# Optimization experiments

Measured on AMD Instinct MI355X. Metric: run time of the kernel, lower is better.

Reference implementation:

```python
import jax, jax.numpy as jnp
import numpy as np

NUM_RBF = 16
MAX_REL = 32          # max_relative_feature
AUTOREGRESSIVE = True
D_MIN, D_MAX = 2.0, 22.0
LN_EPS = 1e-5


def setup_inputs() -> dict:
    key = jax.random.key(0)
    ks = jax.random.split(key, 6)
    B, L, A, K = 1, 1280, 14, 30
    E_feat, edge_in = 128, 16 + NUM_RBF * 4 * 10  # 656
    X = jax.random.normal(ks[0], (B, L, A, 3), dtype=jnp.float32) * 3.0
    residue_idx = jnp.tile(jnp.arange(L, dtype=jnp.int32)[None], (B, 1))
    chain_labels = jnp.zeros((B, L), dtype=jnp.int32)
    E_idx = jax.random.randint(ks[1], (B, L, K), 0, L, dtype=jnp.int32)
    atom_mask = jnp.ones((B, L, A), dtype=jnp.float32)
    W_pos = jax.random.normal(ks[2], (2 * MAX_REL + 2, 16), dtype=jnp.float32) * 0.1
    b_pos = jnp.zeros((16,), dtype=jnp.float32)
    W_edge = jax.random.normal(ks[3], (edge_in, E_feat), dtype=jnp.float32) * 0.05
    ln_gamma = jnp.ones((E_feat,), dtype=jnp.float32)
    ln_beta = jnp.zeros((E_feat,), dtype=jnp.float32)
    return {"X": X, "residue_idx": residue_idx, "chain_labels": chain_labels,
            "E_idx": E_idx, "atom_mask": atom_mask, "W_pos": W_pos,
            "b_pos": b_pos, "W_edge": W_edge, "ln_gamma": ln_gamma,
            "ln_beta": ln_beta}


def _forward(X, residue_idx, chain_labels, E_idx, W_pos, b_pos, W_edge,
             ln_gamma, ln_beta):
    B, L, A, _ = X.shape
    K = E_idx.shape[-1]
    # backbone atoms in loop order [Ca, N, C, O] -> X indices [1, 0, 2, 3]
    bb = X[:, :, jnp.array([1, 0, 2, 3]), :]          # [B, L, 4, 3]
    sc = X[:, :, 4:, :]                               # [B, L, 10, 3]
    Abb = jnp.transpose(bb, (0, 2, 1, 3))             # [B, 4, L, 3]
    Asc = jnp.transpose(sc, (0, 2, 1, 3))             # [B, 10, L, 3]
    # dense pairwise distances for all 40 (bb, sc) atom pairs: [B,4,10,L,L]
    diff = Abb[:, :, None, :, None, :] - Asc[:, None, :, None, :, :]
    D = jnp.sqrt(jnp.sum(diff * diff, axis=-1) + 1e-6)
    # gather top-k neighbor columns -> [B,4,10,L,K]
    D_nb = jnp.take_along_axis(D, E_idx[:, None, None, :, :], axis=4)
    mu = jnp.linspace(D_MIN, D_MAX, NUM_RBF, dtype=D_nb.dtype)
    sigma = (D_MAX - D_MIN) / NUM_RBF
    RBF = jnp.exp(-(((D_nb[..., None] - mu) / sigma) ** 2))  # [B,4,10,L,K,16]
    if AUTOREGRESSIVE:
        self_edges = (E_idx == jnp.arange(L, dtype=E_idx.dtype)[None, :, None])
        RBF = jnp.where(self_edges[:, None, None, :, :, None], 0.0, RBF)
    # concat order: bb outer, sc inner -> [B,L,K, 4*10*16]
    RBF_all = jnp.transpose(RBF, (0, 3, 4, 1, 2, 5)).reshape(B, L, K, 4 * 10 * NUM_RBF)
    # positional encodings
    offset = residue_idx[:, :, None] - residue_idx[:, None, :]        # [B,L,L]
    offset = jnp.take_along_axis(offset, E_idx, axis=2)               # [B,L,K]
    d_chains = (chain_labels[:, :, None] == chain_labels[:, None, :]).astype(jnp.int32)
    E_chains = jnp.take_along_axis(d_chains, E_idx, axis=2)           # [B,L,K]
    d = jnp.clip(offset + MAX_REL, 0, 2 * MAX_REL) * E_chains + (1 - E_chains) * (2 * MAX_REL + 1)
    d_onehot = jax.nn.one_hot(d, 2 * MAX_REL + 2, dtype=W_pos.dtype)  # [B,L,K,66]
    E_positional = d_onehot @ W_pos + b_pos                           # [B,L,K,16]
    E = jnp.concatenate([E_positional, RBF_all], axis=-1)             # [B,L,K,656]
    E = E @ W_edge                                                    # no bias
    # LayerNorm over last dim
    mean = jnp.mean(E, axis=-1, keepdims=True)
    var = jnp.mean((E - mean) ** 2, axis=-1, keepdims=True)
    E = (E - mean) / jnp.sqrt(var + LN_EPS) * ln_gamma + ln_beta
    return E


def reference(X, residue_idx, chain_labels, E_idx, atom_mask, W_pos, b_pos,
              W_edge, ln_gamma, ln_beta):
    E = _forward(X, residue_idx, chain_labels, E_idx, W_pos, b_pos, W_edge,
                 ln_gamma, ln_beta)
    return (E, E_idx)
```

## Files before the change

### kernel.cpp

```cpp
#include <hip/hip_runtime.h>

typedef short bf16x8 __attribute__((ext_vector_type(8)));
typedef float f32x4  __attribute__((ext_vector_type(4)));

#define L_RES 1280
#define A_ATM 14
#define K_NB  30
#define FEAT  656
#define KPAD  672
#define NCH   128
#define WAVES 8
#define AF_STRIDE 680
#define E_OUT_OFF (L_RES * K_NB * NCH)

__device__ __forceinline__ ushort f2bf(float x) {
    union { float f; unsigned u; } v; v.f = x;
    unsigned r = (v.u + 0x7fffu + ((v.u >> 16) & 1u)) >> 16;
    return (ushort)r;
}

__global__ __launch_bounds__(256) void wt_convert_kernel(const float* __restrict__ W,
                                                         ushort* __restrict__ Wt) {
    int idx = blockIdx.x * 256 + threadIdx.x;
    if (idx >= NCH * KPAD) return;
    int n = idx / KPAD, k = idx - n * KPAD;
    float v = (k < FEAT) ? W[k * NCH + n] : 0.0f;
    Wt[idx] = f2bf(v);
}

__global__ __launch_bounds__(512, 6) void sidechain_feat_kernel(
    const float* __restrict__ X,
    const int*   __restrict__ ridx,
    const int*   __restrict__ clab,
    const int*   __restrict__ Eidx,
    const float* __restrict__ Wpos,
    const float* __restrict__ bpos,
    const ushort* __restrict__ Wt,
    const float* __restrict__ gamma,
    const float* __restrict__ beta,
    float* __restrict__ out)
{
    __shared__ __align__(16) ushort Af[32][AF_STRIDE];
    __shared__ __align__(16) float part[32][WAVES][2];

    const int i    = blockIdx.x;
    const int t    = threadIdx.x;
    const int w    = t >> 6;
    const int lane = t & 63;
    const int frow = lane & 15;
    const int quad = lane >> 4;
    const int c0   = w * 16 + frow;

    if (t < K_NB)
        out[E_OUT_OFF + i * K_NB + t] = (float)Eidx[i * K_NB + t];

    const int my_clab = clab[i];
    const int my_ridx = ridx[i];

    if (t < K_NB * 16) {
        int e = t >> 4, c = t & 15;
        int j = Eidx[i * K_NB + e];
        int d;
        if (my_clab == clab[j]) {
            int off = my_ridx - ridx[j] + 32;
            d = off < 0 ? 0 : (off > 64 ? 64 : off);
        } else {
            d = 65;
        }
        Af[e][c] = f2bf(Wpos[d * 16 + c] + bpos[c]);
    }
    if (t < K_NB * 16) Af[t >> 4][FEAT + (t & 15)] = 0;

    const ushort* B0p = Wt + (size_t)c0 * KPAD + quad * 8;
    bf16x8 b0 = *(const bf16x8*)(B0p);
    bf16x8 b1 = *(const bf16x8*)(B0p + 32);
    bf16x8 b2 = *(const bf16x8*)(B0p + 64);
    float gg = gamma[c0], be = beta[c0];

#pragma unroll
    for (int u = 0; u < 3; ++u) {
        int idx = t + u * 512;
        if (idx < K_NB * 40) {
            int e  = idx / 40;
            int p  = idx - e * 40;
            int ab = p / 10, as = p - ab * 10;
            const int perm[4] = {1, 0, 2, 3};
            int j = Eidx[i * K_NB + e];
            const float* xb = X + (size_t)(i * A_ATM + perm[ab]) * 3;
            const float* xp = X + (size_t)(j * A_ATM + 4 + as) * 3;
            float dx = xb[0] - xp[0];
            float dy = xb[1] - xp[1];
            float dz = xb[2] - xp[2];
            float dist = sqrtf(dx * dx + dy * dy + dz * dz + 1e-6f);
            bool self = (j == i);
            unsigned* dst = (unsigned*)&Af[e][16 + p * 16];
#pragma unroll
            for (int q = 0; q < 8; ++q) {
                float m0 = 2.0f + (float)(2 * q)     * (20.0f / 15.0f);
                float m1 = 2.0f + (float)(2 * q + 1) * (20.0f / 15.0f);
                float a0 = (dist - m0) * 0.8f;
                float a1 = (dist - m1) * 0.8f;
                float r0 = self ? 0.0f : __expf(-a0 * a0);
                float r1 = self ? 0.0f : __expf(-a1 * a1);
                unsigned pk;
                asm("v_cvt_pk_bf16_f32 %0, %1, %2" : "=v"(pk) : "v"(r0), "v"(r1));
                dst[q] = pk;
            }
        }
    }
    __syncthreads();

    const ushort* A0p = &Af[frow][quad * 8];
    const ushort* A1p = &Af[16 + frow][quad * 8];
    bf16x8 a0 = *(const bf16x8*)(A0p);
    bf16x8 a1 = *(const bf16x8*)(A1p);

    f32x4 acc0 = {0.f,0.f,0.f,0.f}, acc1 = {0.f,0.f,0.f,0.f};

#pragma unroll
    for (int c = 0; c < 21; ++c) {
        bf16x8 ua0 = a0, ua1 = a1, ub = b0;
        if (c + 1 < 21) {
            a0 = *(const bf16x8*)(A0p + (c + 1) * 32);
            a1 = *(const bf16x8*)(A1p + (c + 1) * 32);
        }
        b0 = b1; b1 = b2;
        if (c + 3 < 21)
            b2 = *(const bf16x8*)(B0p + (c + 3) * 32);
        acc0 = __builtin_amdgcn_mfma_f32_16x16x32_bf16(ua0, ub, acc0, 0, 0, 0);
        acc1 = __builtin_amdgcn_mfma_f32_16x16x32_bf16(ua1, ub, acc1, 0, 0, 0);
    }

    float s0[4], q0[4], s1[4], q1[4];
#pragma unroll
    for (int r = 0; r < 4; ++r) {
        s0[r] = acc0[r];
        q0[r] = acc0[r] * acc0[r];
        s1[r] = acc1[r];
        q1[r] = acc1[r] * acc1[r];
    }
#pragma unroll
    for (int off = 1; off < 16; off <<= 1) {
#pragma unroll
        for (int r = 0; r < 4; ++r) {
            s0[r] += __shfl_xor(s0[r], off);
            q0[r] += __shfl_xor(q0[r], off);
            s1[r] += __shfl_xor(s1[r], off);
            q1[r] += __shfl_xor(q1[r], off);
        }
    }
    if (frow == 0) {
#pragma unroll
        for (int r = 0; r < 4; ++r) {
            int row = quad * 4 + r;
            part[row][w][0]      = s0[r];
            part[row][w][1]      = q0[r];
            part[16 + row][w][0] = s1[r];
            part[16 + row][w][1] = q1[r];
        }
    }
    __syncthreads();

#pragma unroll
    for (int r = 0; r < 4; ++r) {
        int row = quad * 4 + r;
        {
            f32x4 pa = *(const f32x4*)&part[row][0][0];
            f32x4 pb = *(const f32x4*)&part[row][2][0];
            f32x4 pc = *(const f32x4*)&part[row][4][0];
            f32x4 pd = *(const f32x4*)&part[row][6][0];
            float S = pa[0] + pa[2] + pb[0] + pb[2] + pc[0] + pc[2] + pd[0] + pd[2];
            float Q = pa[1] + pa[3] + pb[1] + pb[3] + pc[1] + pc[3] + pd[1] + pd[3];
            float mean = S * (1.0f / 128.0f);
            float rstd = rsqrtf(Q * (1.0f / 128.0f) - mean * mean + 1e-5f);
            out[(size_t)(i * K_NB + row) * NCH + c0] = (acc0[r] - mean) * rstd * gg + be;
        }
        int row1 = 16 + row;
        if (row1 < K_NB) {
            f32x4 pa = *(const f32x4*)&part[row1][0][0];
            f32x4 pb = *(const f32x4*)&part[row1][2][0];
            f32x4 pc = *(const f32x4*)&part[row1][4][0];
            f32x4 pd = *(const f32x4*)&part[row1][6][0];
            float S = pa[0] + pa[2] + pb[0] + pb[2] + pc[0] + pc[2] + pd[0] + pd[2];
            float Q = pa[1] + pa[3] + pb[1] + pb[3] + pc[1] + pc[3] + pd[1] + pd[3];
            float mean = S * (1.0f / 128.0f);
            float rstd = rsqrtf(Q * (1.0f / 128.0f) - mean * mean + 1e-5f);
            out[(size_t)(i * K_NB + row1) * NCH + c0] = (acc1[r] - mean) * rstd * gg + be;
        }
    }
}

extern "C" void kernel_launch(void* const* d_in, const int* in_sizes, int n_in,
                              void* d_out, int out_size, void* d_ws, size_t ws_size,
                              hipStream_t stream) {
    const float* X     = (const float*)d_in[0];
    const int*   ridx  = (const int*)  d_in[1];
    const int*   clab  = (const int*)  d_in[2];
    const int*   Eidx  = (const int*)  d_in[3];
    const float* Wpos  = (const float*)d_in[5];
    const float* bpos  = (const float*)d_in[6];
    const float* Wedge = (const float*)d_in[7];
    const float* gamma = (const float*)d_in[8];
    const float* beta  = (const float*)d_in[9];
    float* out = (float*)d_out;

    ushort* Wt = (ushort*)d_ws;

    wt_convert_kernel<<<(NCH * KPAD + 255) / 256, 256, 0, stream>>>(Wedge, Wt);
    sidechain_feat_kernel<<<L_RES, 512, 0, stream>>>(
        X, ridx, clab, Eidx, Wpos, bpos, Wt, gamma, beta, out);
}
```

Measured before the change: 105.1 us.

## Process five residues per block with double-buffered features and register-resident weights

```diff
diff --git a/kernel.cpp b/kernel.cpp
--- a/kernel.cpp
+++ b/kernel.cpp
@@ -10,7 +10,11 @@
 #define KPAD  672
 #define NCH   128
 #define WAVES 8
+#define RPB   5
+#define NBLK  (L_RES / RPB)
 #define AF_STRIDE 680
+#define AF_BYTES (32 * AF_STRIDE * 2)
+#define LDS_BYTES (2 * AF_BYTES + 2 * 32 * WAVES * 2 * 4)
 #define E_OUT_OFF (L_RES * K_NB * NCH)
 
 __device__ __forceinline__ ushort f2bf(float x) {
@@ -28,7 +32,7 @@
     Wt[idx] = f2bf(v);
 }
 
-__global__ __launch_bounds__(512, 6) void sidechain_feat_kernel(
+__global__ __launch_bounds__(512, 2) void sidechain_feat_kernel(
     const float* __restrict__ X,
     const int*   __restrict__ ridx,
     const int*   __restrict__ clab,
@@ -40,10 +44,11 @@
     const float* __restrict__ beta,
     float* __restrict__ out)
 {
-    __shared__ __align__(16) ushort Af[32][AF_STRIDE];
-    __shared__ __align__(16) float part[32][WAVES][2];
-
-    const int i    = blockIdx.x;
+    extern __shared__ __align__(16) unsigned char smem[];
+    ushort (*Af)[32][AF_STRIDE]  = reinterpret_cast<ushort (*)[32][AF_STRIDE]>(smem);
+    float  (*part)[32][WAVES][2] = reinterpret_cast<float (*)[32][WAVES][2]>(smem + 2 * AF_BYTES);
+
+    const int i0   = blockIdx.x * RPB;
     const int t    = threadIdx.x;
     const int w    = t >> 6;
     const int lane = t & 63;
@@ -51,141 +56,137 @@
     const int quad = lane >> 4;
     const int c0   = w * 16 + frow;
 
-    if (t < K_NB)
-        out[E_OUT_OFF + i * K_NB + t] = (float)Eidx[i * K_NB + t];
-
-    const int my_clab = clab[i];
-    const int my_ridx = ridx[i];
-
-    if (t < K_NB * 16) {
-        int e = t >> 4, c = t & 15;
-        int j = Eidx[i * K_NB + e];
-        int d;
-        if (my_clab == clab[j]) {
-            int off = my_ridx - ridx[j] + 32;
-            d = off < 0 ? 0 : (off > 64 ? 64 : off);
-        } else {
-            d = 65;
-        }
-        Af[e][c] = f2bf(Wpos[d * 16 + c] + bpos[c]);
-    }
-    if (t < K_NB * 16) Af[t >> 4][FEAT + (t & 15)] = 0;
-
     const ushort* B0p = Wt + (size_t)c0 * KPAD + quad * 8;
-    bf16x8 b0 = *(const bf16x8*)(B0p);
-    bf16x8 b1 = *(const bf16x8*)(B0p + 32);
-    bf16x8 b2 = *(const bf16x8*)(B0p + 64);
-    float gg = gamma[c0], be = beta[c0];
-
-#pragma unroll
-    for (int u = 0; u < 3; ++u) {
-        int idx = t + u * 512;
-        if (idx < K_NB * 40) {
-            int e  = idx / 40;
-            int p  = idx - e * 40;
-            int ab = p / 10, as = p - ab * 10;
-            const int perm[4] = {1, 0, 2, 3};
+    bf16x8 B[21];
+#pragma unroll
+    for (int c = 0; c < 21; ++c) B[c] = *(const bf16x8*)(B0p + c * 32);
+    const float gg = gamma[c0], be = beta[c0];
+
+    auto features = [&](int i, int pb) {
+        if (t < K_NB)
+            out[E_OUT_OFF + i * K_NB + t] = (float)Eidx[i * K_NB + t];
+        const int my_clab = clab[i];
+        const int my_ridx = ridx[i];
+        if (t < K_NB * 16) {
+            int e = t >> 4, c = t & 15;
             int j = Eidx[i * K_NB + e];
-            const float* xb = X + (size_t)(i * A_ATM + perm[ab]) * 3;
-            const float* xp = X + (size_t)(j * A_ATM + 4 + as) * 3;
-            float dx = xb[0] - xp[0];
-            float dy = xb[1] - xp[1];
-            float dz = xb[2] - xp[2];
-            float dist = sqrtf(dx * dx + dy * dy + dz * dz + 1e-6f);
-            bool self = (j == i);
-            unsigned* dst = (unsigned*)&Af[e][16 + p * 16];
-#pragma unroll
-            for (int q = 0; q < 8; ++q) {
-                float m0 = 2.0f + (float)(2 * q)     * (20.0f / 15.0f);
-                float m1 = 2.0f + (float)(2 * q + 1) * (20.0f / 15.0f);
-                float a0 = (dist - m0) * 0.8f;
-                float a1 = (dist - m1) * 0.8f;
-                float r0 = self ? 0.0f : __expf(-a0 * a0);
-                float r1 = self ? 0.0f : __expf(-a1 * a1);
-                unsigned pk;
-                asm("v_cvt_pk_bf16_f32 %0, %1, %2" : "=v"(pk) : "v"(r0), "v"(r1));
-                dst[q] = pk;
-            }
-        }
-    }
+            int d;
+            if (my_clab == clab[j]) {
+                int off = my_ridx - ridx[j] + 32;
+                d = off < 0 ? 0 : (off > 64 ? 64 : off);
+            } else {
+                d = 65;
+            }
+            Af[pb][e][c] = f2bf(Wpos[d * 16 + c] + bpos[c]);
+            Af[pb][e][FEAT + c] = 0;
+        }
+#pragma unroll
+        for (int u = 0; u < 3; ++u) {
+            int idx = t + u * 512;
+            if (idx < K_NB * 40) {
+                int e  = idx / 40;
+                int pp = idx - e * 40;
+                int ab = pp / 10, as = pp - ab * 10;
+                const int perm[4] = {1, 0, 2, 3};
+                int j = Eidx[i * K_NB + e];
+                const float* xb = X + (size_t)(i * A_ATM + perm[ab]) * 3;
+                const float* xp = X + (size_t)(j * A_ATM + 4 + as) * 3;
+                float dx = xb[0] - xp[0];
+                float dy = xb[1] - xp[1];
+                float dz = xb[2] - xp[2];
+                float dist = sqrtf(dx * dx + dy * dy + dz * dz + 1e-6f);
+                bool self = (j == i);
+                unsigned* dst = (unsigned*)&Af[pb][e][16 + pp * 16];
+#pragma unroll
+                for (int q = 0; q < 8; ++q) {
+                    float m0 = 2.0f + (float)(2 * q)     * (20.0f / 15.0f);
+                    float m1 = 2.0f + (float)(2 * q + 1) * (20.0f / 15.0f);
+                    float a0 = (dist - m0) * 0.8f;
+                    float a1 = (dist - m1) * 0.8f;
+                    float r0 = self ? 0.0f : __expf(-a0 * a0);
+                    float r1 = self ? 0.0f : __expf(-a1 * a1);
+                    unsigned pk;
+                    asm("v_cvt_pk_bf16_f32 %0, %1, %2" : "=v"(pk) : "v"(r0), "v"(r1));
+                    dst[q] = pk;
+                }
+            }
+        }
+    };
+
+    features(i0, 0);
     __syncthreads();
 
-    const ushort* A0p = &Af[frow][quad * 8];
-    const ushort* A1p = &Af[16 + frow][quad * 8];
-    bf16x8 a0 = *(const bf16x8*)(A0p);
-    bf16x8 a1 = *(const bf16x8*)(A1p);
-
-    f32x4 acc0 = {0.f,0.f,0.f,0.f}, acc1 = {0.f,0.f,0.f,0.f};
-
-#pragma unroll
-    for (int c = 0; c < 21; ++c) {
-        bf16x8 ua0 = a0, ua1 = a1, ub = b0;
-        if (c + 1 < 21) {
-            a0 = *(const bf16x8*)(A0p + (c + 1) * 32);
-            a1 = *(const bf16x8*)(A1p + (c + 1) * 32);
-        }
-        b0 = b1; b1 = b2;
-        if (c + 3 < 21)
-            b2 = *(const bf16x8*)(B0p + (c + 3) * 32);
-        acc0 = __builtin_amdgcn_mfma_f32_16x16x32_bf16(ua0, ub, acc0, 0, 0, 0);
-        acc1 = __builtin_amdgcn_mfma_f32_16x16x32_bf16(ua1, ub, acc1, 0, 0, 0);
-    }
-
-    float s0[4], q0[4], s1[4], q1[4];
-#pragma unroll
-    for (int r = 0; r < 4; ++r) {
-        s0[r] = acc0[r];
-        q0[r] = acc0[r] * acc0[r];
-        s1[r] = acc1[r];
-        q1[r] = acc1[r] * acc1[r];
-    }
-#pragma unroll
-    for (int off = 1; off < 16; off <<= 1) {
+#pragma unroll 1
+    for (int rr = 0; rr < RPB; ++rr) {
+        const int p = rr & 1;
+        if (rr + 1 < RPB) features(i0 + rr + 1, p ^ 1);
+
+        const ushort* A0p = &Af[p][frow][quad * 8];
+        const ushort* A1p = &Af[p][16 + frow][quad * 8];
+        f32x4 acc0 = {0.f,0.f,0.f,0.f}, acc1 = {0.f,0.f,0.f,0.f};
+#pragma unroll
+        for (int c = 0; c < 21; ++c) {
+            bf16x8 a0 = *(const bf16x8*)(A0p + c * 32);
+            bf16x8 a1 = *(const bf16x8*)(A1p + c * 32);
+            acc0 = __builtin_amdgcn_mfma_f32_16x16x32_bf16(a0, B[c], acc0, 0, 0, 0);
+            acc1 = __builtin_amdgcn_mfma_f32_16x16x32_bf16(a1, B[c], acc1, 0, 0, 0);
+        }
+
+        float s0[4], q0[4], s1[4], q1[4];
 #pragma unroll
         for (int r = 0; r < 4; ++r) {
-            s0[r] += __shfl_xor(s0[r], off);
-            q0[r] += __shfl_xor(q0[r], off);
-            s1[r] += __shfl_xor(s1[r], off);
-            q1[r] += __shfl_xor(q1[r], off);
-        }
-    }
-    if (frow == 0) {
+            s0[r] = acc0[r];  q0[r] = acc0[r] * acc0[r];
+            s1[r] = acc1[r];  q1[r] = acc1[r] * acc1[r];
+        }
+#pragma unroll
+        for (int off = 1; off < 16; off <<= 1) {
+#pragma unroll
+            for (int r = 0; r < 4; ++r) {
+                s0[r] += __shfl_xor(s0[r], off);
+                q0[r] += __shfl_xor(q0[r], off);
+                s1[r] += __shfl_xor(s1[r], off);
+                q1[r] += __shfl_xor(q1[r], off);
+            }
+        }
+        if (frow == 0) {
+#pragma unroll
+            for (int r = 0; r < 4; ++r) {
+                int row = quad * 4 + r;
+                part[p][row][w][0]      = s0[r];
+                part[p][row][w][1]      = q0[r];
+                part[p][16 + row][w][0] = s1[r];
+                part[p][16 + row][w][1] = q1[r];
+            }
+        }
+        __syncthreads();
+
+        const int ibase = (i0 + rr) * K_NB;
 #pragma unroll
         for (int r = 0; r < 4; ++r) {
             int row = quad * 4 + r;
-            part[row][w][0]      = s0[r];
-            part[row][w][1]      = q0[r];
-            part[16 + row][w][0] = s1[r];
-            part[16 + row][w][1] = q1[r];
-        }
-    }
-    __syncthreads();
-
-#pragma unroll
-    for (int r = 0; r < 4; ++r) {
-        int row = quad * 4 + r;
-        {
-            f32x4 pa = *(const f32x4*)&part[row][0][0];
-            f32x4 pb = *(const f32x4*)&part[row][2][0];
-            f32x4 pc = *(const f32x4*)&part[row][4][0];
-            f32x4 pd = *(const f32x4*)&part[row][6][0];
-            float S = pa[0] + pa[2] + pb[0] + pb[2] + pc[0] + pc[2] + pd[0] + pd[2];
-            float Q = pa[1] + pa[3] + pb[1] + pb[3] + pc[1] + pc[3] + pd[1] + pd[3];
-            float mean = S * (1.0f / 128.0f);
-            float rstd = rsqrtf(Q * (1.0f / 128.0f) - mean * mean + 1e-5f);
-            out[(size_t)(i * K_NB + row) * NCH + c0] = (acc0[r] - mean) * rstd * gg + be;
-        }
-        int row1 = 16 + row;
-        if (row1 < K_NB) {
-            f32x4 pa = *(const f32x4*)&part[row1][0][0];
-            f32x4 pb = *(const f32x4*)&part[row1][2][0];
-            f32x4 pc = *(const f32x4*)&part[row1][4][0];
-            f32x4 pd = *(const f32x4*)&part[row1][6][0];
-            float S = pa[0] + pa[2] + pb[0] + pb[2] + pc[0] + pc[2] + pd[0] + pd[2];
-            float Q = pa[1] + pa[3] + pb[1] + pb[3] + pc[1] + pc[3] + pd[1] + pd[3];
-            float mean = S * (1.0f / 128.0f);
-            float rstd = rsqrtf(Q * (1.0f / 128.0f) - mean * mean + 1e-5f);
-            out[(size_t)(i * K_NB + row1) * NCH + c0] = (acc1[r] - mean) * rstd * gg + be;
+            {
+                f32x4 pA = *(const f32x4*)&part[p][row][0][0];
+                f32x4 pB = *(const f32x4*)&part[p][row][2][0];
+                f32x4 pC = *(const f32x4*)&part[p][row][4][0];
+                f32x4 pD = *(const f32x4*)&part[p][row][6][0];
+                float S = pA[0]+pA[2]+pB[0]+pB[2]+pC[0]+pC[2]+pD[0]+pD[2];
+                float Q = pA[1]+pA[3]+pB[1]+pB[3]+pC[1]+pC[3]+pD[1]+pD[3];
+                float mean = S * (1.0f / 128.0f);
+                float rstd = rsqrtf(Q * (1.0f / 128.0f) - mean * mean + 1e-5f);
+                out[(size_t)(ibase + row) * NCH + c0] = (acc0[r] - mean) * rstd * gg + be;
+            }
+            int row1 = 16 + row;
+            if (row1 < K_NB) {
+                f32x4 pA = *(const f32x4*)&part[p][row1][0][0];
+                f32x4 pB = *(const f32x4*)&part[p][row1][2][0];
+                f32x4 pC = *(const f32x4*)&part[p][row1][4][0];
+                f32x4 pD = *(const f32x4*)&part[p][row1][6][0];
+                float S = pA[0]+pA[2]+pB[0]+pB[2]+pC[0]+pC[2]+pD[0]+pD[2];
+                float Q = pA[1]+pA[3]+pB[1]+pB[3]+pC[1]+pC[3]+pD[1]+pD[3];
+                float mean = S * (1.0f / 128.0f);
+                float rstd = rsqrtf(Q * (1.0f / 128.0f) - mean * mean + 1e-5f);
+                out[(size_t)(ibase + row1) * NCH + c0] = (acc1[r] - mean) * rstd * gg + be;
+            }
         }
     }
 }
@@ -207,6 +208,6 @@
     ushort* Wt = (ushort*)d_ws;
 
     wt_convert_kernel<<<(NCH * KPAD + 255) / 256, 256, 0, stream>>>(Wedge, Wt);
-    sidechain_feat_kernel<<<L_RES, 512, 0, stream>>>(
+    sidechain_feat_kernel<<<NBLK, 512, LDS_BYTES, stream>>>(
         X, ridx, clab, Eidx, Wpos, bpos, Wt, gamma, beta, out);
 }
```

After: 110.7 us. +5.4%, slower.

## Tile edges globally in groups of 48 to remove padded MFMA rows

Applied to the files above, without the earlier changes.

```diff
diff --git a/kernel.cpp b/kernel.cpp
--- a/kernel.cpp
+++ b/kernel.cpp
@@ -2,10 +2,14 @@
 
 typedef short bf16x8 __attribute__((ext_vector_type(8)));
 typedef float f32x4  __attribute__((ext_vector_type(4)));
+typedef unsigned int u32x4 __attribute__((ext_vector_type(4)));
 
 #define L_RES 1280
 #define A_ATM 14
 #define K_NB  30
+#define NEDGE (L_RES * K_NB)
+#define EPT   48
+#define NBLK  (NEDGE / EPT)
 #define FEAT  656
 #define KPAD  672
 #define NCH   128
@@ -28,7 +32,7 @@
     Wt[idx] = f2bf(v);
 }
 
-__global__ __launch_bounds__(512, 6) void sidechain_feat_kernel(
+__global__ __launch_bounds__(512, 4) void sidechain_feat_kernel(
     const float* __restrict__ X,
     const int*   __restrict__ ridx,
     const int*   __restrict__ clab,
@@ -40,10 +44,10 @@
     const float* __restrict__ beta,
     float* __restrict__ out)
 {
-    __shared__ __align__(16) ushort Af[32][AF_STRIDE];
-    __shared__ __align__(16) float part[32][WAVES][2];
-
-    const int i    = blockIdx.x;
+    __shared__ __align__(16) ushort Af[EPT][AF_STRIDE];
+    __shared__ __align__(16) float part[EPT][WAVES][2];
+
+    const int g0   = blockIdx.x * EPT;
     const int t    = threadIdx.x;
     const int w    = t >> 6;
     const int lane = t & 63;
@@ -51,49 +55,53 @@
     const int quad = lane >> 4;
     const int c0   = w * 16 + frow;
 
-    if (t < K_NB)
-        out[E_OUT_OFF + i * K_NB + t] = (float)Eidx[i * K_NB + t];
-
-    const int my_clab = clab[i];
-    const int my_ridx = ridx[i];
-
-    if (t < K_NB * 16) {
-        int e = t >> 4, c = t & 15;
-        int j = Eidx[i * K_NB + e];
-        int d;
-        if (my_clab == clab[j]) {
-            int off = my_ridx - ridx[j] + 32;
-            d = off < 0 ? 0 : (off > 64 ? 64 : off);
-        } else {
-            d = 65;
-        }
-        Af[e][c] = f2bf(Wpos[d * 16 + c] + bpos[c]);
-    }
-    if (t < K_NB * 16) Af[t >> 4][FEAT + (t & 15)] = 0;
+    if (t < EPT) out[E_OUT_OFF + g0 + t] = (float)Eidx[g0 + t];
 
     const ushort* B0p = Wt + (size_t)c0 * KPAD + quad * 8;
     bf16x8 b0 = *(const bf16x8*)(B0p);
     bf16x8 b1 = *(const bf16x8*)(B0p + 32);
     bf16x8 b2 = *(const bf16x8*)(B0p + 64);
-    float gg = gamma[c0], be = beta[c0];
-
-#pragma unroll
-    for (int u = 0; u < 3; ++u) {
+    const float gg = gamma[c0], be = beta[c0];
+
+#pragma unroll
+    for (int u = 0; u < 2; ++u) {
         int idx = t + u * 512;
-        if (idx < K_NB * 40) {
-            int e  = idx / 40;
-            int p  = idx - e * 40;
-            int ab = p / 10, as = p - ab * 10;
-            const int perm[4] = {1, 0, 2, 3};
-            int j = Eidx[i * K_NB + e];
-            const float* xb = X + (size_t)(i * A_ATM + perm[ab]) * 3;
+        if (idx < EPT * 16) {
+            int eg = idx >> 4, c = idx & 15;
+            int g = g0 + eg;
+            int i = g / K_NB;
+            int j = Eidx[g];
+            int d;
+            if (clab[i] == clab[j]) {
+                int off = ridx[i] - ridx[j] + 32;
+                d = off < 0 ? 0 : (off > 64 ? 64 : off);
+            } else {
+                d = 65;
+            }
+            Af[eg][c] = f2bf(Wpos[d * 16 + c] + bpos[c]);
+            Af[eg][FEAT + c] = 0;
+        }
+    }
+
+#pragma unroll
+    for (int u = 0; u < 4; ++u) {
+        int idx = t + u * 512;
+        if (idx < EPT * 40) {
+            int eg = idx % EPT;
+            int pr = idx / EPT;
+            int g = g0 + eg;
+            int i = g / K_NB;
+            int j = Eidx[g];
+            int ab = pr / 10, as = pr - ab * 10;
+            int pa = ab < 2 ? 1 - ab : ab;
+            const float* xb = X + (size_t)(i * A_ATM + pa) * 3;
             const float* xp = X + (size_t)(j * A_ATM + 4 + as) * 3;
             float dx = xb[0] - xp[0];
             float dy = xb[1] - xp[1];
             float dz = xb[2] - xp[2];
             float dist = sqrtf(dx * dx + dy * dy + dz * dz + 1e-6f);
             bool self = (j == i);
-            unsigned* dst = (unsigned*)&Af[e][16 + p * 16];
+            unsigned pk[8];
 #pragma unroll
             for (int q = 0; q < 8; ++q) {
                 float m0 = 2.0f + (float)(2 * q)     * (20.0f / 15.0f);
@@ -102,92 +110,89 @@
                 float a1 = (dist - m1) * 0.8f;
                 float r0 = self ? 0.0f : __expf(-a0 * a0);
                 float r1 = self ? 0.0f : __expf(-a1 * a1);
-                unsigned pk;
-                asm("v_cvt_pk_bf16_f32 %0, %1, %2" : "=v"(pk) : "v"(r0), "v"(r1));
-                dst[q] = pk;
-            }
+                asm("v_cvt_pk_bf16_f32 %0, %1, %2" : "=v"(pk[q]) : "v"(r0), "v"(r1));
+            }
+            u32x4* dst = (u32x4*)&Af[eg][16 + pr * 16];
+            u32x4 v0 = {pk[0], pk[1], pk[2], pk[3]};
+            u32x4 v1 = {pk[4], pk[5], pk[6], pk[7]};
+            dst[0] = v0;
+            dst[1] = v1;
         }
     }
     __syncthreads();
 
     const ushort* A0p = &Af[frow][quad * 8];
     const ushort* A1p = &Af[16 + frow][quad * 8];
-    bf16x8 a0 = *(const bf16x8*)(A0p);
-    bf16x8 a1 = *(const bf16x8*)(A1p);
-
-    f32x4 acc0 = {0.f,0.f,0.f,0.f}, acc1 = {0.f,0.f,0.f,0.f};
+    const ushort* A2p = &Af[32 + frow][quad * 8];
+    bf16x8 a0 = *(const bf16x8*)A0p;
+    bf16x8 a1 = *(const bf16x8*)A1p;
+    bf16x8 a2 = *(const bf16x8*)A2p;
+
+    f32x4 acc0 = {0.f,0.f,0.f,0.f}, acc1 = {0.f,0.f,0.f,0.f}, acc2 = {0.f,0.f,0.f,0.f};
 
 #pragma unroll
     for (int c = 0; c < 21; ++c) {
-        bf16x8 ua0 = a0, ua1 = a1, ub = b0;
+        bf16x8 ua0 = a0, ua1 = a1, ua2 = a2, ub = b0;
         if (c + 1 < 21) {
             a0 = *(const bf16x8*)(A0p + (c + 1) * 32);
             a1 = *(const bf16x8*)(A1p + (c + 1) * 32);
+            a2 = *(const bf16x8*)(A2p + (c + 1) * 32);
         }
         b0 = b1; b1 = b2;
         if (c + 3 < 21)
             b2 = *(const bf16x8*)(B0p + (c + 3) * 32);
         acc0 = __builtin_amdgcn_mfma_f32_16x16x32_bf16(ua0, ub, acc0, 0, 0, 0);
         acc1 = __builtin_amdgcn_mfma_f32_16x16x32_bf16(ua1, ub, acc1, 0, 0, 0);
-    }
-
-    float s0[4], q0[4], s1[4], q1[4];
+        acc2 = __builtin_amdgcn_mfma_f32_16x16x32_bf16(ua2, ub, acc2, 0, 0, 0);
+    }
+
+    float s[3][4], q[3][4];
 #pragma unroll
     for (int r = 0; r < 4; ++r) {
-        s0[r] = acc0[r];
-        q0[r] = acc0[r] * acc0[r];
-        s1[r] = acc1[r];
-        q1[r] = acc1[r] * acc1[r];
+        s[0][r] = acc0[r];  q[0][r] = acc0[r] * acc0[r];
+        s[1][r] = acc1[r];  q[1][r] = acc1[r] * acc1[r];
+        s[2][r] = acc2[r];  q[2][r] = acc2[r] * acc2[r];
     }
 #pragma unroll
     for (int off = 1; off < 16; off <<= 1) {
 #pragma unroll
+        for (int m = 0; m < 3; ++m)
+#pragma unroll
+            for (int r = 0; r < 4; ++r) {
+                s[m][r] += __shfl_xor(s[m][r], off);
+                q[m][r] += __shfl_xor(q[m][r], off);
+            }
+    }
+    if (frow == 0) {
+#pragma unroll
+        for (int m = 0; m < 3; ++m)
+#pragma unroll
+            for (int r = 0; r < 4; ++r) {
+                int row = m * 16 + quad * 4 + r;
+                part[row][w][0] = s[m][r];
+                part[row][w][1] = q[m][r];
+            }
+    }
+    __syncthreads();
+
+    auto finalize = [&](const f32x4& acc, int m) {
+#pragma unroll
         for (int r = 0; r < 4; ++r) {
-            s0[r] += __shfl_xor(s0[r], off);
-            q0[r] += __shfl_xor(q0[r], off);
-            s1[r] += __shfl_xor(s1[r], off);
-            q1[r] += __shfl_xor(q1[r], off);
-        }
-    }
-    if (frow == 0) {
-#pragma unroll
-        for (int r = 0; r < 4; ++r) {
-            int row = quad * 4 + r;
-            part[row][w][0]      = s0[r];
-            part[row][w][1]      = q0[r];
-            part[16 + row][w][0] = s1[r];
-            part[16 + row][w][1] = q1[r];
-        }
-    }
-    __syncthreads();
-
-#pragma unroll
-    for (int r = 0; r < 4; ++r) {
-        int row = quad * 4 + r;
-        {
-            f32x4 pa = *(const f32x4*)&part[row][0][0];
-            f32x4 pb = *(const f32x4*)&part[row][2][0];
-            f32x4 pc = *(const f32x4*)&part[row][4][0];
-            f32x4 pd = *(const f32x4*)&part[row][6][0];
-            float S = pa[0] + pa[2] + pb[0] + pb[2] + pc[0] + pc[2] + pd[0] + pd[2];
-            float Q = pa[1] + pa[3] + pb[1] + pb[3] + pc[1] + pc[3] + pd[1] + pd[3];
+            int row = m * 16 + quad * 4 + r;
+            f32x4 pA = *(const f32x4*)&part[row][0][0];
+            f32x4 pB = *(const f32x4*)&part[row][2][0];
+            f32x4 pC = *(const f32x4*)&part[row][4][0];
+            f32x4 pD = *(const f32x4*)&part[row][6][0];
+            float S = pA[0]+pA[2]+pB[0]+pB[2]+pC[0]+pC[2]+pD[0]+pD[2];
+            float Q = pA[1]+pA[3]+pB[1]+pB[3]+pC[1]+pC[3]+pD[1]+pD[3];
             float mean = S * (1.0f / 128.0f);
             float rstd = rsqrtf(Q * (1.0f / 128.0f) - mean * mean + 1e-5f);
-            out[(size_t)(i * K_NB + row) * NCH + c0] = (acc0[r] - mean) * rstd * gg + be;
-        }
-        int row1 = 16 + row;
-        if (row1 < K_NB) {
-            f32x4 pa = *(const f32x4*)&part[row1][0][0];
-            f32x4 pb = *(const f32x4*)&part[row1][2][0];
-            f32x4 pc = *(const f32x4*)&part[row1][4][0];
-            f32x4 pd = *(const f32x4*)&part[row1][6][0];
-            float S = pa[0] + pa[2] + pb[0] + pb[2] + pc[0] + pc[2] + pd[0] + pd[2];
-            float Q = pa[1] + pa[3] + pb[1] + pb[3] + pc[1] + pc[3] + pd[1] + pd[3];
-            float mean = S * (1.0f / 128.0f);
-            float rstd = rsqrtf(Q * (1.0f / 128.0f) - mean * mean + 1e-5f);
-            out[(size_t)(i * K_NB + row1) * NCH + c0] = (acc1[r] - mean) * rstd * gg + be;
-        }
-    }
+            out[(size_t)(g0 + row) * NCH + c0] = (acc[r] - mean) * rstd * gg + be;
+        }
+    };
+    finalize(acc0, 0);
+    finalize(acc1, 1);
+    finalize(acc2, 2);
 }
 
 extern "C" void kernel_launch(void* const* d_in, const int* in_sizes, int n_in,
@@ -207,6 +212,6 @@
     ushort* Wt = (ushort*)d_ws;
 
     wt_convert_kernel<<<(NCH * KPAD + 255) / 256, 256, 0, stream>>>(Wedge, Wt);
-    sidechain_feat_kernel<<<L_RES, 512, 0, stream>>>(
+    sidechain_feat_kernel<<<NBLK, 512, 0, stream>>>(
         X, ridx, clab, Eidx, Wpos, bpos, Wt, gamma, beta, out);
 }
```

Result: slower. 109.2 us (+3.9%).
